# Performance work log

Measured on AMD Instinct MI355X. Metric: run time of the kernel, lower is better.

Reference implementation:

```python
import jax, jax.numpy as jnp
import numpy as np

B, I, A_IN = 32, 32, 16     # batch, input capsules, input atoms
OD, OA = 10, 16             # output_dim (classes), output_atoms
H, W = 12, 12               # spatial grid
NUM_ROUTING = 3


def _squash(t):
    # squash over atom dim (axis=2): x/|x| * |x|^2/(1+|x|^2) = x*|x|/(1+|x|^2)
    norm = jnp.linalg.norm(t, axis=2, keepdims=True)
    return t * norm / (1.0 + norm * norm)


def setup_inputs() -> dict:
    key = jax.random.key(0)
    k1, k2 = jax.random.split(key)
    x = jax.random.normal(k1, (B, I, A_IN, H, W), dtype=jnp.float32)
    # torch weight: (I, A_IN, OD*OA, 1, 1), init N(0, 0.1)
    weight = 0.1 * jax.random.normal(k2, (I, A_IN, OD * OA), dtype=jnp.float32)
    # torch bias: (OD, OA, 1, 1), init const 0.1
    bias = jnp.full((OD, OA, 1, 1), 0.1, dtype=jnp.float32)
    return {"x": x, "weight": weight, "bias": bias}


def reference(x, weight, bias):
    # votes: sum over input atoms -> [B, I, OD*OA, H, W] -> [B, I, OD, OA, H, W]
    votes = jnp.einsum("biahw,iak->bikhw", x, weight)
    votes = votes.reshape(B, I, OD, OA, H, W)
    biases = jnp.broadcast_to(bias, (OD, OA, H, W))

    # Dynamic routing. In the original, logits carry no gradient (built from
    # .data), so intermediate iterations are fully stop-gradient.
    votes_sg = jax.lax.stop_gradient(votes)
    logits = jnp.zeros((B, I, OD, H, W), dtype=votes.dtype)
    activation = None
    for i in range(NUM_ROUTING):
        route = jax.nn.softmax(logits, axis=2)  # softmax over output_dim
        v = votes if i == NUM_ROUTING - 1 else votes_sg
        preact = jnp.einsum("bidhw,bidahw->bdahw", route, v) + biases
        activation = _squash(preact)  # [B, OD, OA, H, W]
        if i < NUM_ROUTING - 1:
            # agreement (dot over atoms) updates logits
            logits = logits + jnp.einsum(
                "bidahw,bdahw->bidhw", votes_sg, jax.lax.stop_gradient(activation)
            )
    return activation
```

## Files before the change

kernel.cpp:

```cpp
#include <hip/hip_runtime.h>
#include <math.h>

#define NB 32
#define NI 32
#define NA 16
#define NOD 10
#define NOA 16
#define NK 160
#define NHW 144
#define NROUT 3
#define NROWS (NB*NHW)
#define SVLD 168

#define XT_OFF 262144
#define WS_NEEDED (XT_OFF + (size_t)NROWS * 512 * 4)

__device__ __forceinline__ unsigned short f2bf(float f) {
    unsigned b = __builtin_bit_cast(unsigned, f);
    b += 0x7fffu + ((b >> 16) & 1u);
    return (unsigned short)(b >> 16);
}
__device__ __forceinline__ float bf_lo(unsigned d) {
    return __builtin_bit_cast(float, d << 16);
}
__device__ __forceinline__ float bf_hi(unsigned d) {
    return __builtin_bit_cast(float, d & 0xffff0000u);
}

__global__ __launch_bounds__(256)
void prepass_kernel(const float* __restrict__ x,
                    const float* __restrict__ weight,
                    unsigned short* __restrict__ w_bf,
                    float* __restrict__ x_t)
{
    int bid = blockIdx.x;
    const int tid = threadIdx.x;
    if (bid < 320) {
        const int idx = bid * 256 + tid;
        w_bf[idx] = f2bf(weight[idx]);
        return;
    }
    bid -= 320;
    const int b  = bid / 72;
    const int r  = bid % 72;
    const int jt = r / 9;
    const int ht = r % 9;
    const int j0 = jt * 64, hw0 = ht * 16;

    __shared__ float tile[64][17];
    {
        const int hh = tid & 15;
        const int j1 = tid >> 4;
#pragma unroll
        for (int s = 0; s < 4; ++s) {
            const int jj = j1 + s * 16;
            tile[jj][hh] = x[(size_t)b * 73728 + (size_t)(j0 + jj) * NHW + hw0 + hh];
        }
    }
    __syncthreads();
    {
        const int jj = tid >> 2;
        const int p  = tid & 3;
#pragma unroll
        for (int s = 0; s < 4; ++s) {
            const int hwg = ht * 4 + s;
            x_t[((size_t)b * 36 + hwg) * 2048 + (size_t)(j0 + jj) * 4 + p] =
                tile[jj][s * 4 + p];
        }
    }
}

__global__ __launch_bounds__(512, 4)
void capsule_fused5_kernel(const float* __restrict__ x_t,
                           const unsigned short* __restrict__ w_bf,
                           const float* __restrict__ bias,
                           float* __restrict__ out)
{
    __shared__ unsigned short sv[4][NI][SVLD];
    __shared__ __align__(16) float smem[2696];
    float* const slog_f         = smem;
    unsigned short* const srt_h = (unsigned short*)(smem + 1360);
    float* const sact_f         = smem + 2040;
    float* const xp             = smem;

    const int tid = threadIdx.x;
    const int wid = tid >> 6;
    const int l   = tid & 63;
    const int w2  = wid >> 1;
    const int hf  = wid & 1;
    const int b   = blockIdx.x / (NHW / 4);
    const int hw0 = (blockIdx.x % (NHW / 4)) * 4;

    {
        const float4* src = reinterpret_cast<const float4*>(x_t + (size_t)blockIdx.x * 2048);
        reinterpret_cast<float4*>(xp)[tid] = src[tid];
    }
    __syncthreads();

    for (int t = tid; t < NI * 40; t += 512) {
        const int i  = t / 40;
        const int kq = t - i * 40;
        const int k0 = kq * 4;
        const unsigned short* wp = w_bf + (size_t)i * NA * NK + k0;
        float4 a0 = make_float4(0.f, 0.f, 0.f, 0.f);
        float4 a1 = a0, a2 = a0, a3 = a0;
#pragma unroll
        for (int a = 0; a < NA; ++a) {
            const uint2 wv = *reinterpret_cast<const uint2*>(wp + (size_t)a * NK);
            const float w0 = bf_lo(wv.x), w1 = bf_hi(wv.x);
            const float w2_ = bf_lo(wv.y), w3 = bf_hi(wv.y);
            const float4 xa = *reinterpret_cast<const float4*>(&xp[(i * NA + a) * 4]);
            a0.x = fmaf(xa.x, w0, a0.x); a0.y = fmaf(xa.x, w1, a0.y);
            a0.z = fmaf(xa.x, w2_, a0.z); a0.w = fmaf(xa.x, w3, a0.w);
            a1.x = fmaf(xa.y, w0, a1.x); a1.y = fmaf(xa.y, w1, a1.y);
            a1.z = fmaf(xa.y, w2_, a1.z); a1.w = fmaf(xa.y, w3, a1.w);
            a2.x = fmaf(xa.z, w0, a2.x); a2.y = fmaf(xa.z, w1, a2.y);
            a2.z = fmaf(xa.z, w2_, a2.z); a2.w = fmaf(xa.z, w3, a2.w);
            a3.x = fmaf(xa.w, w0, a3.x); a3.y = fmaf(xa.w, w1, a3.y);
            a3.z = fmaf(xa.w, w2_, a3.z); a3.w = fmaf(xa.w, w3, a3.w);
        }
        *reinterpret_cast<ushort4*>(&sv[0][i][k0]) =
            make_ushort4(f2bf(a0.x), f2bf(a0.y), f2bf(a0.z), f2bf(a0.w));
        *reinterpret_cast<ushort4*>(&sv[1][i][k0]) =
            make_ushort4(f2bf(a1.x), f2bf(a1.y), f2bf(a1.z), f2bf(a1.w));
        *reinterpret_cast<ushort4*>(&sv[2][i][k0]) =
            make_ushort4(f2bf(a2.x), f2bf(a2.y), f2bf(a2.z), f2bf(a2.w));
        *reinterpret_cast<ushort4*>(&sv[3][i][k0]) =
            make_ushort4(f2bf(a3.x), f2bf(a3.y), f2bf(a3.z), f2bf(a3.w));
    }

    const int kb = hf * 80;
    const int ob = hf * 5;
    int kq = 0, hh = 0, odg = 0, kg = 0;
    float4 bq = make_float4(0.f, 0.f, 0.f, 0.f);
    if (l < 40) {
        kq  = l >> 1;
        hh  = l & 1;
        odg = ob + (kq >> 2);
        kg  = kb + kq * 4;
        if (hh == 0)
            bq = *reinterpret_cast<const float4*>(bias + kg);
    }
    const int li = l & 31;

    float lgp[3] = {0.f, 0.f, 0.f};

    __syncthreads();

    for (int it = 0; it < NROUT; ++it) {
        if (it > 0) {
            float e[NOD];
            float m = -1e30f;
#pragma unroll
            for (int od = 0; od < NOD; ++od) {
                e[od] = slog_f[(w2 * NOD + od) * 34 + li];
                m = fmaxf(m, e[od]);
            }
            float s = 0.f;
#pragma unroll
            for (int od = 0; od < NOD; ++od) {
                e[od] = __expf(e[od] - m);
                s += e[od];
            }
            const float inv = 1.f / s;
            if (l < 32) {
#pragma unroll
                for (int odl = 0; odl < 5; ++odl)
                    srt_h[(w2 * NOD + ob + odl) * 34 + li] = f2bf(e[ob + odl] * inv);
            }
            __syncthreads();
        }

        if (l < 40) {
            float a0 = bq.x, a1 = bq.y, a2 = bq.z, a3 = bq.w;
            const unsigned short* svb  = &sv[w2][hh * 16][kg];
            const unsigned short* srow = &srt_h[(w2 * NOD + odg) * 34 + hh * 16];
#pragma unroll
            for (int s2 = 0; s2 < 8; ++s2) {
                float r0, r1;
                if (it == 0) {
                    r0 = 0.1f; r1 = 0.1f;
                } else {
                    const unsigned u = *reinterpret_cast<const unsigned*>(srow + 2 * s2);
                    r0 = bf_lo(u); r1 = bf_hi(u);
                }
                const uint2 d0 = *reinterpret_cast<const uint2*>(svb + (2 * s2) * SVLD);
                const uint2 d1 = *reinterpret_cast<const uint2*>(svb + (2 * s2 + 1) * SVLD);
                a0 = fmaf(r0, bf_lo(d0.x), a0);
                a1 = fmaf(r0, bf_hi(d0.x), a1);
                a2 = fmaf(r0, bf_lo(d0.y), a2);
                a3 = fmaf(r0, bf_hi(d0.y), a3);
                a0 = fmaf(r1, bf_lo(d1.x), a0);
                a1 = fmaf(r1, bf_hi(d1.x), a1);
                a2 = fmaf(r1, bf_lo(d1.y), a2);
                a3 = fmaf(r1, bf_hi(d1.y), a3);
            }
            a0 += __shfl_xor(a0, 1, 2);
            a1 += __shfl_xor(a1, 1, 2);
            a2 += __shfl_xor(a2, 1, 2);
            a3 += __shfl_xor(a3, 1, 2);
            float ss = a0 * a0 + a1 * a1 + a2 * a2 + a3 * a3;
            ss += __shfl_xor(ss, 2, 8);
            ss += __shfl_xor(ss, 4, 8);
            const float sc = sqrtf(ss) / (1.f + ss);
            if (hh == 0)
                *reinterpret_cast<float4*>(&sact_f[w2 * 164 + kg]) =
                    make_float4(a0 * sc, a1 * sc, a2 * sc, a3 * sc);
        }
        __builtin_amdgcn_wave_barrier();

        if (it < NROUT - 1) {
#pragma unroll
            for (int r = 0; r < 3; ++r) {
                const int t = l + 64 * r;
                if (t < 160) {
                    const int odl = t >> 5;
                    const int i   = t & 31;
                    const int od  = ob + odl;
                    const int kk  = od * 16;
                    const uint4 d0 = *reinterpret_cast<const uint4*>(&sv[w2][i][kk]);
                    const uint4 d1 = *reinterpret_cast<const uint4*>(&sv[w2][i][kk + 8]);
                    const float* ap = &sact_f[w2 * 164 + kk];
                    const float4 c0 = *reinterpret_cast<const float4*>(ap + 0);
                    const float4 c1 = *reinterpret_cast<const float4*>(ap + 4);
                    const float4 c2 = *reinterpret_cast<const float4*>(ap + 8);
                    const float4 c3 = *reinterpret_cast<const float4*>(ap + 12);
                    float acc;
                    acc  = bf_lo(d0.x) * c0.x;
                    acc = fmaf(bf_hi(d0.x), c0.y, acc);
                    acc = fmaf(bf_lo(d0.y), c0.z, acc);
                    acc = fmaf(bf_hi(d0.y), c0.w, acc);
                    acc = fmaf(bf_lo(d0.z), c1.x, acc);
                    acc = fmaf(bf_hi(d0.z), c1.y, acc);
                    acc = fmaf(bf_lo(d0.w), c1.z, acc);
                    acc = fmaf(bf_hi(d0.w), c1.w, acc);
                    acc = fmaf(bf_lo(d1.x), c2.x, acc);
                    acc = fmaf(bf_hi(d1.x), c2.y, acc);
                    acc = fmaf(bf_lo(d1.y), c2.z, acc);
                    acc = fmaf(bf_hi(d1.y), c2.w, acc);
                    acc = fmaf(bf_lo(d1.z), c3.x, acc);
                    acc = fmaf(bf_hi(d1.z), c3.y, acc);
                    acc = fmaf(bf_lo(d1.w), c3.z, acc);
                    acc = fmaf(bf_hi(d1.w), c3.w, acc);
                    lgp[r] += acc;
                    slog_f[(w2 * NOD + od) * 34 + i] = lgp[r];
                }
            }
            __syncthreads();
        }
    }

    __syncthreads();
    if (tid < NK) {
        const float4 v = make_float4(sact_f[0 * 164 + tid], sact_f[1 * 164 + tid],
                                     sact_f[2 * 164 + tid], sact_f[3 * 164 + tid]);
        *reinterpret_cast<float4*>(out + ((size_t)b * NK + tid) * NHW + hw0) = v;
    }
}

__global__ __launch_bounds__(256)
void capsule_fused_kernel(const float* __restrict__ x,
                          const float* __restrict__ weight,
                          const float* __restrict__ bias,
                          float* __restrict__ out)
{
    __shared__ unsigned short sv[4][NI][SVLD];
    __shared__ __align__(16) float pool[2048];
    float* const srt_f  = pool;
    float* const sact_f = pool + 4 * NOD * 33;

    const int tid = threadIdx.x;
    const int w   = tid >> 6;
    const int l   = tid & 63;
    const int b   = blockIdx.x / (NHW / 4);
    const int hw0 = (blockIdx.x % (NHW / 4)) * 4;

    {
        const float* xb = x + ((size_t)b * NI * NA) * NHW + hw0;
        for (int j = tid; j < NI * NA; j += 256) {
            const float4 v = *reinterpret_cast<const float4*>(xb + (size_t)j * NHW);
            *reinterpret_cast<float4*>(&pool[j * 4]) = v;
        }
    }
    __syncthreads();

    for (int j = tid; j < NI * 40; j += 256) {
        const int i  = j / 40;
        const int kq = j - i * 40;
        const int k0 = kq * 4;
        const float4* wp = reinterpret_cast<const float4*>(weight + (size_t)i * NA * NK + k0);
        float4 a0 = make_float4(0.f,0.f,0.f,0.f), a1 = a0, a2 = a0, a3 = a0;
#pragma unroll
        for (int a = 0; a < NA; ++a) {
            const float4 w4 = wp[(size_t)a * 40];
            const float4 xa = *reinterpret_cast<const float4*>(&pool[(i * NA + a) * 4]);
            a0.x = fmaf(xa.x, w4.x, a0.x); a0.y = fmaf(xa.x, w4.y, a0.y);
            a0.z = fmaf(xa.x, w4.z, a0.z); a0.w = fmaf(xa.x, w4.w, a0.w);
            a1.x = fmaf(xa.y, w4.x, a1.x); a1.y = fmaf(xa.y, w4.y, a1.y);
            a1.z = fmaf(xa.y, w4.z, a1.z); a1.w = fmaf(xa.y, w4.w, a1.w);
            a2.x = fmaf(xa.z, w4.x, a2.x); a2.y = fmaf(xa.z, w4.y, a2.y);
            a2.z = fmaf(xa.z, w4.z, a2.z); a2.w = fmaf(xa.z, w4.w, a2.w);
            a3.x = fmaf(xa.w, w4.x, a3.x); a3.y = fmaf(xa.w, w4.y, a3.y);
            a3.z = fmaf(xa.w, w4.z, a3.z); a3.w = fmaf(xa.w, w4.w, a3.w);
        }
        *reinterpret_cast<ushort4*>(&sv[0][i][k0]) =
            make_ushort4(f2bf(a0.x), f2bf(a0.y), f2bf(a0.z), f2bf(a0.w));
        *reinterpret_cast<ushort4*>(&sv[1][i][k0]) =
            make_ushort4(f2bf(a1.x), f2bf(a1.y), f2bf(a1.z), f2bf(a1.w));
        *reinterpret_cast<ushort4*>(&sv[2][i][k0]) =
            make_ushort4(f2bf(a2.x), f2bf(a2.y), f2bf(a2.z), f2bf(a2.w));
        *reinterpret_cast<ushort4*>(&sv[3][i][k0]) =
            make_ushort4(f2bf(a3.x), f2bf(a3.y), f2bf(a3.z), f2bf(a3.w));
    }

    const float2 b0 = *reinterpret_cast<const float2*>(bias + 2 * l);
    float2 b1 = make_float2(0.f, 0.f);
    if (l < 16) b1 = *reinterpret_cast<const float2*>(bias + 128 + 2 * l);

    float lg[NOD];
#pragma unroll
    for (int od = 0; od < NOD; ++od) lg[od] = 0.f;
    const int iown = l & 31;

    __syncthreads();

    for (int it = 0; it < NROUT; ++it) {
        {
            float m = lg[0];
#pragma unroll
            for (int od = 1; od < NOD; ++od) m = fmaxf(m, lg[od]);
            float e[NOD];
            float s = 0.f;
#pragma unroll
            for (int od = 0; od < NOD; ++od) { e[od] = __expf(lg[od] - m); s += e[od]; }
            const float inv = 1.f / s;
            if (l < 32) {
#pragma unroll
                for (int od = 0; od < NOD; ++od)
                    srt_f[(w * NOD + od) * 33 + iown] = e[od] * inv;
            }
        }
        __builtin_amdgcn_wave_barrier();
        {
            const int od0 = l >> 3;
            float a0 = b0.x, a1 = b0.y;
#pragma unroll
            for (int i = 0; i < NI; ++i) {
                const unsigned d = *reinterpret_cast<const unsigned*>(&sv[w][i][2 * l]);
                const float r = srt_f[(w * NOD + od0) * 33 + i];
                a0 = fmaf(r, bf_lo(d), a0);
                a1 = fmaf(r, bf_hi(d), a1);
            }
            float ss = a0 * a0 + a1 * a1;
            ss += __shfl_xor(ss, 1, 8);
            ss += __shfl_xor(ss, 2, 8);
            ss += __shfl_xor(ss, 4, 8);
            const float sc = sqrtf(ss) / (1.f + ss);
            *reinterpret_cast<float2*>(&sact_f[w * 164 + 2 * l]) = make_float2(a0 * sc, a1 * sc);
            if (l < 16) {
                const int od1 = 8 + (l >> 3);
                float c0 = b1.x, c1 = b1.y;
#pragma unroll
                for (int i = 0; i < NI; ++i) {
                    const unsigned d = *reinterpret_cast<const unsigned*>(&sv[w][i][128 + 2 * l]);
                    const float r = srt_f[(w * NOD + od1) * 33 + i];
                    c0 = fmaf(r, bf_lo(d), c0);
                    c1 = fmaf(r, bf_hi(d), c1);
                }
                float s2 = c0 * c0 + c1 * c1;
                s2 += __shfl_xor(s2, 1, 8);
                s2 += __shfl_xor(s2, 2, 8);
                s2 += __shfl_xor(s2, 4, 8);
                const float sc2 = sqrtf(s2) / (1.f + s2);
                *reinterpret_cast<float2*>(&sact_f[w * 164 + 128 + 2 * l]) =
                    make_float2(c0 * sc2, c1 * sc2);
            }
        }
        __builtin_amdgcn_wave_barrier();
        if (it < NROUT - 1) {
#pragma unroll
            for (int r = 0; r < 5; ++r) {
                const int t  = l + 64 * r;
                const int i  = t & 31;
                const int od = t >> 5;
                const uint4 d0 = *reinterpret_cast<const uint4*>(&sv[w][i][od * NOA]);
                const uint4 d1 = *reinterpret_cast<const uint4*>(&sv[w][i][od * NOA + 8]);
                const float* ap = &sact_f[w * 164 + od * NOA];
                const float4 c0 = *reinterpret_cast<const float4*>(ap + 0);
                const float4 c1 = *reinterpret_cast<const float4*>(ap + 4);
                const float4 c2 = *reinterpret_cast<const float4*>(ap + 8);
                const float4 c3 = *reinterpret_cast<const float4*>(ap + 12);
                float acc;
                acc  = bf_lo(d0.x) * c0.x;
                acc = fmaf(bf_hi(d0.x), c0.y, acc);
                acc = fmaf(bf_lo(d0.y), c0.z, acc);
                acc = fmaf(bf_hi(d0.y), c0.w, acc);
                acc = fmaf(bf_lo(d0.z), c1.x, acc);
                acc = fmaf(bf_hi(d0.z), c1.y, acc);
                acc = fmaf(bf_lo(d0.w), c1.z, acc);
                acc = fmaf(bf_hi(d0.w), c1.w, acc);
                acc = fmaf(bf_lo(d1.x), c2.x, acc);
                acc = fmaf(bf_hi(d1.x), c2.y, acc);
                acc = fmaf(bf_lo(d1.y), c2.z, acc);
                acc = fmaf(bf_hi(d1.y), c2.w, acc);
                acc = fmaf(bf_lo(d1.z), c3.x, acc);
                acc = fmaf(bf_hi(d1.z), c3.y, acc);
                acc = fmaf(bf_lo(d1.w), c3.z, acc);
                acc = fmaf(bf_hi(d1.w), c3.w, acc);
                srt_f[(w * NOD + od) * 33 + i] = acc;
            }
            __builtin_amdgcn_wave_barrier();
#pragma unroll
            for (int od = 0; od < NOD; ++od)
                lg[od] += srt_f[(w * NOD + od) * 33 + iown];
            __builtin_amdgcn_wave_barrier();
        }
    }

    __syncthreads();
    if (tid < NK) {
        const float4 v = make_float4(sact_f[0 * 164 + tid], sact_f[1 * 164 + tid],
                                     sact_f[2 * 164 + tid], sact_f[3 * 164 + tid]);
        *reinterpret_cast<float4*>(out + ((size_t)b * NK + tid) * NHW + hw0) = v;
    }
}

extern "C" void kernel_launch(void* const* d_in, const int* in_sizes, int n_in,
                              void* d_out, int out_size, void* d_ws, size_t ws_size,
                              hipStream_t stream) {
    const float* x      = (const float*)d_in[0];
    const float* weight = (const float*)d_in[1];
    const float* bias   = (const float*)d_in[2];
    float* out          = (float*)d_out;

    if (ws_size >= WS_NEEDED) {
        unsigned short* w_bf = (unsigned short*)d_ws;
        float* x_t = (float*)((char*)d_ws + XT_OFF);
        prepass_kernel<<<320 + NB * 72, 256, 0, stream>>>(x, weight, w_bf, x_t);
        capsule_fused5_kernel<<<NROWS / 4, 512, 0, stream>>>(x_t, w_bf, bias, out);
    } else {
        capsule_fused_kernel<<<NB * (NHW / 4), 256, 0, stream>>>(x, weight, bias, out);
    }
}
```

Measured before the change: 48.97 us.

## Halve spatial positions per block and double-buffer bf16 logits

The fused capsule kernel now handles 2 spatial positions per 256-thread block instead of 4 per 512-thread block, which doubles the grid and shrinks shared memory so more blocks fit per CU. The prepass writes x_t in a layout with 2 positions per group to match. Routing logits are stored in bf16 in a double-buffered shared array, so the barrier after the softmax becomes a wave barrier. In exchange, each block recomputes the votes setup, and the logits carry lower precision.

```diff
diff --git a/kernel.cpp b/kernel.cpp
--- a/kernel.cpp
+++ b/kernel.cpp
@@ -19,6 +19,9 @@
     unsigned b = __builtin_bit_cast(unsigned, f);
     b += 0x7fffu + ((b >> 16) & 1u);
     return (unsigned short)(b >> 16);
+}
+__device__ __forceinline__ float bf2f(unsigned short u) {
+    return __builtin_bit_cast(float, (unsigned)u << 16);
 }
 __device__ __forceinline__ float bf_lo(unsigned d) {
     return __builtin_bit_cast(float, d << 16);
@@ -59,82 +62,75 @@
     }
     __syncthreads();
     {
-        const int jj = tid >> 2;
-        const int p  = tid & 3;
-#pragma unroll
-        for (int s = 0; s < 4; ++s) {
-            const int hwg = ht * 4 + s;
-            x_t[((size_t)b * 36 + hwg) * 2048 + (size_t)(j0 + jj) * 4 + p] =
-                tile[jj][s * 4 + p];
-        }
-    }
-}
-
-__global__ __launch_bounds__(512, 4)
-void capsule_fused5_kernel(const float* __restrict__ x_t,
+        const int jj = tid & 63;
+        const int q  = tid >> 6;
+#pragma unroll
+        for (int s = 0; s < 2; ++s) {
+            const int pp = q + 4 * s;
+            const float2 v = make_float2(tile[jj][2 * pp], tile[jj][2 * pp + 1]);
+            *reinterpret_cast<float2*>(
+                &x_t[(((size_t)b * 72 + ht * 8 + pp) * 512 + j0 + jj) * 2]) = v;
+        }
+    }
+}
+
+__global__ __launch_bounds__(256, 8)
+void capsule_fused6_kernel(const float* __restrict__ x_t,
                            const unsigned short* __restrict__ w_bf,
                            const float* __restrict__ bias,
                            float* __restrict__ out)
 {
-    __shared__ unsigned short sv[4][NI][SVLD];
-    __shared__ __align__(16) float smem[2696];
-    float* const slog_f         = smem;
-    unsigned short* const srt_h = (unsigned short*)(smem + 1360);
-    float* const sact_f         = smem + 2040;
-    float* const xp             = smem;
+    __shared__ unsigned short sv[2][NI][SVLD];
+    __shared__ __align__(16) float smem[1348];
+    unsigned short* const slog_h = (unsigned short*)smem;
+    unsigned short* const srt_h  = (unsigned short*)(smem + 680);
+    float* const sact_f          = smem + 1020;
+    float* const xp              = smem;
 
     const int tid = threadIdx.x;
     const int wid = tid >> 6;
     const int l   = tid & 63;
     const int w2  = wid >> 1;
     const int hf  = wid & 1;
-    const int b   = blockIdx.x / (NHW / 4);
-    const int hw0 = (blockIdx.x % (NHW / 4)) * 4;
+    const int b   = blockIdx.x / 72;
+    const int hw0 = (blockIdx.x % 72) * 2;
 
     {
-        const float4* src = reinterpret_cast<const float4*>(x_t + (size_t)blockIdx.x * 2048);
-        reinterpret_cast<float4*>(xp)[tid] = src[tid];
-    }
-    __syncthreads();
-
-    for (int t = tid; t < NI * 40; t += 512) {
+        reinterpret_cast<float4*>(xp)[tid] =
+            reinterpret_cast<const float4*>(x_t + (size_t)blockIdx.x * 1024)[tid];
+    }
+    __syncthreads();
+
+    for (int t = tid; t < NI * 40; t += 256) {
         const int i  = t / 40;
         const int kq = t - i * 40;
         const int k0 = kq * 4;
         const unsigned short* wp = w_bf + (size_t)i * NA * NK + k0;
         float4 a0 = make_float4(0.f, 0.f, 0.f, 0.f);
-        float4 a1 = a0, a2 = a0, a3 = a0;
+        float4 a1 = a0;
 #pragma unroll
         for (int a = 0; a < NA; ++a) {
             const uint2 wv = *reinterpret_cast<const uint2*>(wp + (size_t)a * NK);
             const float w0 = bf_lo(wv.x), w1 = bf_hi(wv.x);
             const float w2_ = bf_lo(wv.y), w3 = bf_hi(wv.y);
-            const float4 xa = *reinterpret_cast<const float4*>(&xp[(i * NA + a) * 4]);
+            const float2 xa = *reinterpret_cast<const float2*>(&xp[(i * NA + a) * 2]);
             a0.x = fmaf(xa.x, w0, a0.x); a0.y = fmaf(xa.x, w1, a0.y);
             a0.z = fmaf(xa.x, w2_, a0.z); a0.w = fmaf(xa.x, w3, a0.w);
             a1.x = fmaf(xa.y, w0, a1.x); a1.y = fmaf(xa.y, w1, a1.y);
             a1.z = fmaf(xa.y, w2_, a1.z); a1.w = fmaf(xa.y, w3, a1.w);
-            a2.x = fmaf(xa.z, w0, a2.x); a2.y = fmaf(xa.z, w1, a2.y);
-            a2.z = fmaf(xa.z, w2_, a2.z); a2.w = fmaf(xa.z, w3, a2.w);
-            a3.x = fmaf(xa.w, w0, a3.x); a3.y = fmaf(xa.w, w1, a3.y);
-            a3.z = fmaf(xa.w, w2_, a3.z); a3.w = fmaf(xa.w, w3, a3.w);
         }
         *reinterpret_cast<ushort4*>(&sv[0][i][k0]) =
             make_ushort4(f2bf(a0.x), f2bf(a0.y), f2bf(a0.z), f2bf(a0.w));
         *reinterpret_cast<ushort4*>(&sv[1][i][k0]) =
             make_ushort4(f2bf(a1.x), f2bf(a1.y), f2bf(a1.z), f2bf(a1.w));
-        *reinterpret_cast<ushort4*>(&sv[2][i][k0]) =
-            make_ushort4(f2bf(a2.x), f2bf(a2.y), f2bf(a2.z), f2bf(a2.w));
-        *reinterpret_cast<ushort4*>(&sv[3][i][k0]) =
-            make_ushort4(f2bf(a3.x), f2bf(a3.y), f2bf(a3.z), f2bf(a3.w));
     }
 
     const int kb = hf * 80;
     const int ob = hf * 5;
-    int kq = 0, hh = 0, odg = 0, kg = 0;
+    int hh = 0, odg = 0, kg = 0;
     float4 bq = make_float4(0.f, 0.f, 0.f, 0.f);
     if (l < 40) {
-        kq  = l >> 1;
+        const int kq = l >> 1;
         hh  = l & 1;
         odg = ob + (kq >> 2);
         kg  = kb + kq * 4;
@@ -149,11 +145,12 @@
 
     for (int it = 0; it < NROUT; ++it) {
         if (it > 0) {
+            const int rbuf = it & 1;
             float e[NOD];
             float m = -1e30f;
 #pragma unroll
             for (int od = 0; od < NOD; ++od) {
-                e[od] = slog_f[(w2 * NOD + od) * 34 + li];
+                e[od] = bf2f(slog_h[((rbuf * 2 + w2) * NOD + od) * 34 + li]);
                 m = fmaxf(m, e[od]);
             }
             float s = 0.f;
@@ -166,9 +163,9 @@
             if (l < 32) {
 #pragma unroll
                 for (int odl = 0; odl < 5; ++odl)
-                    srt_h[(w2 * NOD + ob + odl) * 34 + li] = f2bf(e[ob + odl] * inv);
-            }
-            __syncthreads();
+                    srt_h[((w2 * NOD) + ob + odl) * 34 + li] = f2bf(e[ob + odl] * inv);
+            }
+            __builtin_amdgcn_wave_barrier();
         }
 
         if (l < 40) {
@@ -210,6 +207,7 @@
         __builtin_amdgcn_wave_barrier();
 
         if (it < NROUT - 1) {
+            const int wbuf = (it + 1) & 1;
 #pragma unroll
             for (int r = 0; r < 3; ++r) {
                 const int t = l + 64 * r;
@@ -243,7 +241,7 @@
                     acc = fmaf(bf_lo(d1.w), c3.z, acc);
                     acc = fmaf(bf_hi(d1.w), c3.w, acc);
                     lgp[r] += acc;
-                    slog_f[(w2 * NOD + od) * 34 + i] = lgp[r];
+                    slog_h[((wbuf * 2 + w2) * NOD + od) * 34 + i] = f2bf(lgp[r]);
                 }
             }
             __syncthreads();
@@ -252,9 +250,8 @@
 
     __syncthreads();
     if (tid < NK) {
-        const float4 v = make_float4(sact_f[0 * 164 + tid], sact_f[1 * 164 + tid],
-                                     sact_f[2 * 164 + tid], sact_f[3 * 164 + tid]);
-        *reinterpret_cast<float4*>(out + ((size_t)b * NK + tid) * NHW + hw0) = v;
+        const float2 v = make_float2(sact_f[tid], sact_f[164 + tid]);
+        *reinterpret_cast<float2*>(out + ((size_t)b * NK + tid) * NHW + hw0) = v;
     }
 }
 
@@ -437,7 +434,7 @@
         unsigned short* w_bf = (unsigned short*)d_ws;
         float* x_t = (float*)((char*)d_ws + XT_OFF);
         prepass_kernel<<<320 + NB * 72, 256, 0, stream>>>(x, weight, w_bf, x_t);
-        capsule_fused5_kernel<<<NROWS / 4, 512, 0, stream>>>(x_t, w_bf, bias, out);
+        capsule_fused6_kernel<<<NROWS / 2, 256, 0, stream>>>(x_t, w_bf, bias, out);
     } else {
         capsule_fused_kernel<<<NB * (NHW / 4), 256, 0, stream>>>(x, weight, bias, out);
     }
```

New measurement: 51.58 us. 1.05x slower.
